# Optimization experiments

Hardware: AMD Instinct MI355X
Metric: run time of the kernel (lower is better)

Reference implementation:

```python
import jax, jax.numpy as jnp
import numpy as np

ALPHA = 1.0
K = 5          # kernel height == width
STRIDE = 1


def extract_patches(x, k, stride):
    """x: (N, C, H, W) -> (N, k*k*C, Ho, Wo), feature order (kh, kw, c)
    to match k.view(kh*kw*C, F) flattening of a (kh, kw, C, F) kernel."""
    p = jax.lax.conv_general_dilated_patches(x, (k, k), (stride, stride), 'VALID')
    N, _, Ho, Wo = p.shape
    C = x.shape[1]
    # conv_general_dilated_patches is channel-major: (C, kh, kw) -> reorder to (kh, kw, C)
    p = p.reshape(N, C, k, k, Ho, Wo).transpose(0, 2, 3, 1, 4, 5)
    return p.reshape(N, k * k * C, Ho, Wo)


def setup_inputs():
    key = jax.random.key(0)
    kx, kk1, kk2 = jax.random.split(key, 3)
    N, C, H, W = 8, 4, 64, 64
    F = 16
    # xavier-uniform-ish scale for kernels
    limit = float(np.sqrt(6.0 / (K * K * C + F)))
    x = jax.random.normal(kx, (N, C, H, W), jnp.float32)
    k1 = jax.random.uniform(kk1, (K, K, C, F), jnp.float32, -limit, limit)
    k2 = jax.random.uniform(kk2, (K, K, C, F), jnp.float32, -limit, limit)
    bias = jnp.zeros((F,), jnp.float32)
    return {"x": x, "k1": k1, "k2": k2, "bias": bias}


def _smooth_max(patches, kflat):
    # patches: (N, P, Ho, Wo); kflat: (P, F)
    z = patches[:, :, None] + kflat[None, :, :, None, None]  # (N, P, F, Ho, Wo)
    w = jax.nn.softmax(ALPHA * z, axis=1)  # exp(alpha*z)/sum over patch dim (stable)
    return jnp.sum(z * w, axis=1)          # (N, F, Ho, Wo)


def reference(x, k1, k2, bias):
    kh, kw, C, F = k1.shape
    patches = extract_patches(x, kh, STRIDE)        # (N, kh*kw*C, Ho, Wo)
    y11 = _smooth_max(patches, k1.reshape(-1, F))   # smooth-max of  x + k1
    y21 = _smooth_max(-patches, k2.reshape(-1, F))  # smooth-max of -x + k2
    return y11 + y21 + bias[None, :, None, None]
```

## Files before the change

### kernel.cpp

```cpp
#include <hip/hip_runtime.h>

#define NN 8
#define CC 4
#define HH 64
#define WW 64
#define KK 5
#define FF 16
#define HO 60
#define WO 60
#define PP (KK * KK * CC)

typedef float v4f __attribute__((ext_vector_type(4)));
typedef float v2f __attribute__((ext_vector_type(2)));

__global__ __launch_bounds__(512) void smorph_fused(
        const float* __restrict__ x, const float* __restrict__ k1,
        const float* __restrict__ k2, const float* __restrict__ bias,
        float* __restrict__ out) {
    __shared__ v4f pq[CC * KK * 64 + 4];
    __shared__ v4f wlds[PP * 16];
    __shared__ v2f red[4 * 8 * 64];

    int b = blockIdx.x;
    int n = b / HO;
    int ho = b - n * HO;
    int t = threadIdx.x;

    for (int i = t; i < PP * 16; i += 512) {
        int p = i >> 4, rem = i & 15, side = rem >> 3, f2 = rem & 7;
        const float* kp = side ? k2 : k1;
        float ka = kp[p * FF + 2 * f2];
        float kb = kp[p * FF + 2 * f2 + 1];
        float ea = __expf(ka), eb = __expf(kb);
        v4f wv = {ea, eb, ka * ea, kb * eb};
        wlds[i] = wv;
    }
    for (int i = t; i < CC * KK * 64; i += 512) {
        int w = i & 63;
        int cr = i >> 6;
        int c = cr / KK, r = cr - c * KK;
        float v = x[((n * CC + c) * HH + (ho + r)) * WW + w];
        float e1 = __expf(v), e2 = __expf(-v);
        v4f qv = {e1, v * e1, e2, -v * e2};
        pq[i] = qv;
    }
    __syncthreads();

    int lane = t & 63;
    int wid = t >> 6;
    int fg = wid & 3;
    int ch = wid >> 2;
    int fp2 = fg * 2;

    v2f d1[2], n1[2], d2[2], n2[2];
#pragma unroll
    for (int jj = 0; jj < 2; ++jj) {
        d1[jj] = 0.f; n1[jj] = 0.f; d2[jj] = 0.f; n2[jj] = 0.f;
    }

#pragma unroll 1
    for (int ci = 0; ci < 2; ++ci) {
        int c = ch * 2 + ci;
#pragma unroll
        for (int kh = 0; kh < KK; ++kh) {
            const v4f* prow = &pq[(c * KK + kh) * 64 + lane];
#pragma unroll
            for (int kw = 0; kw < KK; ++kw) {
                v4f q = prow[kw];
                const v4f* wp = &wlds[((kh * KK + kw) * CC + c) * 16 + fp2];
#pragma unroll
                for (int jp = 0; jp < 2; ++jp) {
                    v4f w1 = wp[jp];
                    v4f w2 = wp[8 + jp];
                    d1[jp] += q.xx * w1.xy;
                    n1[jp] += q.yy * w1.xy + q.xx * w1.zw;
                    d2[jp] += q.zz * w2.xy;
                    n2[jp] += q.ww * w2.xy + q.zz * w2.zw;
                }
            }
        }
    }

    v2f* rr = &red[fg * 8 * 64 + lane];
    if (ch) {
        rr[0 * 64] = d1[0]; rr[1 * 64] = d1[1];
        rr[2 * 64] = n1[0]; rr[3 * 64] = n1[1];
        rr[4 * 64] = d2[0]; rr[5 * 64] = d2[1];
        rr[6 * 64] = n2[0]; rr[7 * 64] = n2[1];
    }
    __syncthreads();
    if (!ch && lane < WO) {
        d1[0] += rr[0 * 64]; d1[1] += rr[1 * 64];
        n1[0] += rr[2 * 64]; n1[1] += rr[3 * 64];
        d2[0] += rr[4 * 64]; d2[1] += rr[5 * 64];
        n2[0] += rr[6 * 64]; n2[1] += rr[7 * 64];
#pragma unroll
        for (int jp = 0; jp < 2; ++jp) {
            v2f o = n1[jp] / d1[jp] + n2[jp] / d2[jp];
            int f0 = fg * 4 + 2 * jp;
            out[((size_t)(n * FF + f0) * HO + ho) * WO + lane] = o.x + bias[f0];
            out[((size_t)(n * FF + f0 + 1) * HO + ho) * WO + lane] =
                o.y + bias[f0 + 1];
        }
    }
}

extern "C" void kernel_launch(void* const* d_in, const int* in_sizes, int n_in,
                              void* d_out, int out_size, void* d_ws, size_t ws_size,
                              hipStream_t stream) {
    const float* x    = (const float*)d_in[0];
    const float* k1   = (const float*)d_in[1];
    const float* k2   = (const float*)d_in[2];
    const float* bias = (const float*)d_in[3];
    float* out = (float*)d_out;

    smorph_fused<<<480, 512, 0, stream>>>(x, k1, k2, bias, out);
}
```

Before: 70.82 us.

## Precompute weight exponentials in separate kernel and split channels across 1024 threads

Moves the per-block exp(k) weight table construction into a small preceding kernel that writes to workspace, so each conv block reads weights from global/L2 instead of rebuilding them in LDS. The conv block grows to 1024 threads with one channel per wave group, and partial sums are reduced through a three-slot LDS buffer. It also preloads the five patch values per kernel row into registers. This adds a second kernel launch, relies on cached global weight loads, and may raise register pressure at 1024 threads.

```diff
diff --git a/kernel.cpp b/kernel.cpp
--- a/kernel.cpp
+++ b/kernel.cpp
@@ -13,29 +13,32 @@
 typedef float v4f __attribute__((ext_vector_type(4)));
 typedef float v2f __attribute__((ext_vector_type(2)));
 
-__global__ __launch_bounds__(512) void smorph_fused(
-        const float* __restrict__ x, const float* __restrict__ k1,
-        const float* __restrict__ k2, const float* __restrict__ bias,
-        float* __restrict__ out) {
+__global__ void smorph_weights(const float* __restrict__ k1,
+                               const float* __restrict__ k2,
+                               float4* __restrict__ wq) {
+    int i = blockIdx.x * blockDim.x + threadIdx.x;
+    if (i < PP * FF) {
+        int p = i >> 4, rem = i & 15, side = rem >> 3, f2 = rem & 7;
+        const float* kp = side ? k2 : k1;
+        float ka = kp[p * FF + 2 * f2];
+        float kb = kp[p * FF + 2 * f2 + 1];
+        float ea = __expf(ka), eb = __expf(kb);
+        wq[i] = make_float4(ea, eb, ka * ea, kb * eb);
+    }
+}
+
+__global__ __launch_bounds__(1024) void smorph_conv(
+        const float* __restrict__ x, const v4f* __restrict__ wq,
+        const float* __restrict__ bias, float* __restrict__ out) {
     __shared__ v4f pq[CC * KK * 64 + 4];
-    __shared__ v4f wlds[PP * 16];
-    __shared__ v2f red[4 * 8 * 64];
+    __shared__ v2f red[3][4][8][64];
 
     int b = blockIdx.x;
     int n = b / HO;
     int ho = b - n * HO;
     int t = threadIdx.x;
 
-    for (int i = t; i < PP * 16; i += 512) {
-        int p = i >> 4, rem = i & 15, side = rem >> 3, f2 = rem & 7;
-        const float* kp = side ? k2 : k1;
-        float ka = kp[p * FF + 2 * f2];
-        float kb = kp[p * FF + 2 * f2 + 1];
-        float ea = __expf(ka), eb = __expf(kb);
-        v4f wv = {ea, eb, ka * ea, kb * eb};
-        wlds[i] = wv;
-    }
-    for (int i = t; i < CC * KK * 64; i += 512) {
+    for (int i = t; i < CC * KK * 64; i += 1024) {
         int w = i & 63;
         int cr = i >> 6;
         int c = cr / KK, r = cr - c * KK;
@@ -49,8 +52,7 @@
     int lane = t & 63;
     int wid = t >> 6;
     int fg = wid & 3;
-    int ch = wid >> 2;
-    int fp2 = fg * 2;
+    int cw = wid >> 2;
 
     v2f d1[2], n1[2], d2[2], n2[2];
 #pragma unroll
@@ -58,42 +60,46 @@
         d1[jj] = 0.f; n1[jj] = 0.f; d2[jj] = 0.f; n2[jj] = 0.f;
     }
 
-#pragma unroll 1
-    for (int ci = 0; ci < 2; ++ci) {
-        int c = ch * 2 + ci;
 #pragma unroll
-        for (int kh = 0; kh < KK; ++kh) {
-            const v4f* prow = &pq[(c * KK + kh) * 64 + lane];
+    for (int kh = 0; kh < KK; ++kh) {
+        const v4f* prow = &pq[(cw * KK + kh) * 64 + lane];
+        v4f q[KK];
 #pragma unroll
-            for (int kw = 0; kw < KK; ++kw) {
-                v4f q = prow[kw];
-                const v4f* wp = &wlds[((kh * KK + kw) * CC + c) * 16 + fp2];
+        for (int kw = 0; kw < KK; ++kw) q[kw] = prow[kw];
 #pragma unroll
-                for (int jp = 0; jp < 2; ++jp) {
-                    v4f w1 = wp[jp];
-                    v4f w2 = wp[8 + jp];
-                    d1[jp] += q.xx * w1.xy;
-                    n1[jp] += q.yy * w1.xy + q.xx * w1.zw;
-                    d2[jp] += q.zz * w2.xy;
-                    n2[jp] += q.ww * w2.xy + q.zz * w2.zw;
-                }
-            }
+        for (int kw = 0; kw < KK; ++kw) {
+            const v4f* wp = wq + ((kh * KK + kw) * CC + cw) * 16 + fg * 2;
+            v4f w1a = wp[0], w1b = wp[1];
+            v4f w2a = wp[8], w2b = wp[9];
+            v4f qv = q[kw];
+            d1[0] += qv.xx * w1a.xy;
+            n1[0] += qv.yy * w1a.xy + qv.xx * w1a.zw;
+            d1[1] += qv.xx * w1b.xy;
+            n1[1] += qv.yy * w1b.xy + qv.xx * w1b.zw;
+            d2[0] += qv.zz * w2a.xy;
+            n2[0] += qv.ww * w2a.xy + qv.zz * w2a.zw;
+            d2[1] += qv.zz * w2b.xy;
+            n2[1] += qv.ww * w2b.xy + qv.zz * w2b.zw;
         }
     }
 
-    v2f* rr = &red[fg * 8 * 64 + lane];
-    if (ch) {
+    if (cw) {
+        v2f* rr = &red[cw - 1][fg][0][lane];
         rr[0 * 64] = d1[0]; rr[1 * 64] = d1[1];
         rr[2 * 64] = n1[0]; rr[3 * 64] = n1[1];
         rr[4 * 64] = d2[0]; rr[5 * 64] = d2[1];
         rr[6 * 64] = n2[0]; rr[7 * 64] = n2[1];
     }
     __syncthreads();
-    if (!ch && lane < WO) {
-        d1[0] += rr[0 * 64]; d1[1] += rr[1 * 64];
-        n1[0] += rr[2 * 64]; n1[1] += rr[3 * 64];
-        d2[0] += rr[4 * 64]; d2[1] += rr[5 * 64];
-        n2[0] += rr[6 * 64]; n2[1] += rr[7 * 64];
+    if (!cw && lane < WO) {
+#pragma unroll
+        for (int r = 0; r < 3; ++r) {
+            const v2f* rr = &red[r][fg][0][lane];
+            d1[0] += rr[0 * 64]; d1[1] += rr[1 * 64];
+            n1[0] += rr[2 * 64]; n1[1] += rr[3 * 64];
+            d2[0] += rr[4 * 64]; d2[1] += rr[5 * 64];
+            n2[0] += rr[6 * 64]; n2[1] += rr[7 * 64];
+        }
 #pragma unroll
         for (int jp = 0; jp < 2; ++jp) {
             v2f o = n1[jp] / d1[jp] + n2[jp] / d2[jp];
@@ -114,5 +120,8 @@
     const float* bias = (const float*)d_in[3];
     float* out = (float*)d_out;
 
-    smorph_fused<<<480, 512, 0, stream>>>(x, k1, k2, bias, out);
+    float4* wqf = (float4*)d_ws;
+
+    smorph_weights<<<(PP * FF + 255) / 256, 256, 0, stream>>>(k1, k2, wqf);
+    smorph_conv<<<480, 1024, 0, stream>>>(x, (const v4f*)d_ws, bias, out);
 }
```

New measurement: 87.22 us. +23.1%, slower.
